# Kernel optimization log

Hardware: AMD Instinct MI355X
Metric: run time of the kernel (lower is better)

The kernel has to match this reference:

```python
import jax, jax.numpy as jnp
import numpy as np

B, CQ, CKV, H, W = 8, 256, 512, 64, 64
HKV, WKV = 32, 32
DQK = CQ // 8  # 32


def setup_inputs() -> dict:
    key = jax.random.key(0)
    ks = jax.random.split(key, 9)
    s = 0.05
    return {
        "query": jax.random.normal(ks[0], (B, CQ, H, W), jnp.float32),
        "key_value": jax.random.normal(ks[1], (B, CKV, HKV, WKV), jnp.float32),
        "Wq": jax.random.normal(ks[2], (DQK, CQ), jnp.float32) * s,
        "bq": jax.random.normal(ks[3], (DQK,), jnp.float32) * s,
        "Wk": jax.random.normal(ks[4], (DQK, CKV), jnp.float32) * s,
        "bk": jax.random.normal(ks[5], (DQK,), jnp.float32) * s,
        "Wv": jax.random.normal(ks[6], (CQ, CKV), jnp.float32) * s,
        "bv": jax.random.normal(ks[7], (CQ,), jnp.float32) * s,
        "gamma": jax.random.normal(ks[8], (1,), jnp.float32) * 0.5,
    }


def reference(query, key_value, Wq, bq, Wk, bk, Wv, bv, gamma):
    b, cq, h, w = query.shape
    n = h * w
    # bilinear resize of key_value to query's spatial size (align_corners=False
    # half-pixel convention, matching torch F.interpolate and jax.image.resize)
    kv = jax.image.resize(key_value, (b, key_value.shape[1], h, w), method="bilinear")
    # 1x1 convs are channel contractions
    q = jnp.einsum("bchw,dc->bdhw", query, Wq) + bq[None, :, None, None]   # [B,DQK,H,W]
    k = jnp.einsum("bchw,dc->bdhw", kv, Wk) + bk[None, :, None, None]      # [B,DQK,H,W]
    v = jnp.einsum("bchw,dc->bdhw", kv, Wv) + bv[None, :, None, None]      # [B,CQ,H,W]
    qf = q.reshape(b, -1, n)   # [B,DQK,N]
    kf = k.reshape(b, -1, n)   # [B,DQK,N]
    vf = v.reshape(b, -1, n)   # [B,CQ,N]
    energy = jnp.einsum("bdn,bdm->bnm", qf, kf)        # [B,N,N]
    attention = jax.nn.softmax(energy, axis=-1)
    out = jnp.einsum("bnm,bcm->bcn", attention, vf)     # [B,CQ,N]
    out = out.reshape(b, cq, h, w)
    return gamma[0] * out + query
```

## Files before the change

### kernel.cpp

```cpp
#include <hip/hip_runtime.h>

#define B_ 8
#define CQ_ 256
#define CKV_ 512
#define N_ 4096
#define DQK_ 32

typedef __bf16 bf16;
typedef __bf16 bf16x4 __attribute__((ext_vector_type(4)));
typedef __bf16 bf16x8 __attribute__((ext_vector_type(8)));
typedef float f32x4 __attribute__((ext_vector_type(4)));

__global__ void k_convert_w(const float* __restrict__ Wq, const float* __restrict__ Wk,
                            const float* __restrict__ Wv,
                            bf16* __restrict__ wq, bf16* __restrict__ wk, bf16* __restrict__ wv) {
    int i = blockIdx.x * 256 + threadIdx.x;
    if (i < 8192) wq[i] = (bf16)Wq[i];
    else if (i < 24576) wk[i - 8192] = (bf16)Wk[i - 8192];
    else if (i < 155648) wv[i - 24576] = (bf16)Wv[i - 24576];
}

__global__ __launch_bounds__(256) void k_resize(const float* __restrict__ kv, bf16* __restrict__ kvr) {
    const int yo = blockIdx.x;
    const int b  = blockIdx.y;
    const int tid = threadIdx.x;
    __shared__ float r0[64][33];
    __shared__ float r1[64][33];
    int ty = yo >> 1;
    int y0, y1; float wy0, wy1;
    if ((yo & 1) == 0) { y0 = ty > 0 ? ty - 1 : 0; y1 = ty; wy0 = 0.25f; wy1 = 0.75f; }
    else               { y0 = ty; y1 = ty < 31 ? ty + 1 : 31; wy0 = 0.75f; wy1 = 0.25f; }
    const int u_loc = tid & 63;
    const int xo_base = tid >> 6;
    for (int uc = 0; uc < CKV_; uc += 64) {
        __syncthreads();
        for (int i = 0; i < 8; ++i) {
            int idx = tid + i * 256;
            int u = idx >> 5, x = idx & 31;
            const float* src = kv + ((size_t)b * CKV_ + uc + u) * 1024 + x;
            r0[u][x] = src[y0 * 32];
            r1[u][x] = src[y1 * 32];
        }
        __syncthreads();
        for (int i = 0; i < 16; ++i) {
            int xo = xo_base + i * 4;
            int tx = xo >> 1;
            int xa, xb; float wxa, wxb;
            if ((xo & 1) == 0) { xa = tx > 0 ? tx - 1 : 0; xb = tx; wxa = 0.25f; wxb = 0.75f; }
            else               { xa = tx; xb = tx < 31 ? tx + 1 : 31; wxa = 0.75f; wxb = 0.25f; }
            float v0 = wxa * r0[u_loc][xa] + wxb * r0[u_loc][xb];
            float v1 = wxa * r1[u_loc][xa] + wxb * r1[u_loc][xb];
            float val = wy0 * v0 + wy1 * v1;
            kvr[((size_t)b * N_ + yo * 64 + xo) * CKV_ + uc + u_loc] = (bf16)val;
        }
    }
}

__global__ __launch_bounds__(256) void k_proj_q_fused(const float* __restrict__ query,
                                                      const bf16* __restrict__ W,
                                                      const float* __restrict__ bias,
                                                      bf16* __restrict__ qTb) {
    __shared__ bf16 tile[64][264];
    const int n0 = blockIdx.x * 64;
    const int b  = blockIdx.y;
    const int tid = threadIdx.x;
    const int xi = tid & 15, c0 = tid >> 4;
    for (int pass = 0; pass < 16; ++pass) {
        int c = c0 + pass * 16;
        const float4 v = *(const float4*)(query + ((size_t)b * CQ_ + c) * N_ + n0 + xi * 4);
        tile[xi * 4 + 0][c] = (bf16)v.x;
        tile[xi * 4 + 1][c] = (bf16)v.y;
        tile[xi * 4 + 2][c] = (bf16)v.z;
        tile[xi * 4 + 3][c] = (bf16)v.w;
    }
    __syncthreads();
    const int w = tid >> 6, lane = tid & 63;
    const int l16 = lane & 15, quad = lane >> 4;
    const int ct = w & 1, nh = w >> 1;
    f32x4 acc[2];
    acc[0] = (f32x4){0.f, 0.f, 0.f, 0.f}; acc[1] = (f32x4){0.f, 0.f, 0.f, 0.f};
    const bf16* aptr = W + (ct * 16 + l16) * CQ_ + quad * 8;
#pragma unroll
    for (int ks = 0; ks < 8; ++ks) {
        bf16x8 af = *(const bf16x8*)(aptr + ks * 32);
        for (int j = 0; j < 2; ++j) {
            bf16x8 bfv = *(const bf16x8*)&tile[nh * 32 + j * 16 + l16][ks * 32 + quad * 8];
            acc[j] = __builtin_amdgcn_mfma_f32_16x16x32_bf16(af, bfv, acc[j], 0, 0, 0);
        }
    }
    for (int j = 0; j < 2; ++j)
        for (int r = 0; r < 4; ++r) {
            int d = ct * 16 + quad * 4 + r;
            int n = n0 + nh * 32 + j * 16 + l16;
            qTb[((size_t)b * N_ + n) * DQK_ + d] = (bf16)(acc[j][r] + bias[d]);
        }
}

__global__ __launch_bounds__(256) void k_proj_k(const bf16* __restrict__ W,
                                                const float* __restrict__ bias,
                                                const bf16* __restrict__ Bm,
                                                bf16* __restrict__ outT) {
    const int mb = blockIdx.x * 128;
    const int b  = blockIdx.y;
    const int tid = threadIdx.x;
    const int w = tid >> 6, lane = tid & 63;
    const int l16 = lane & 15, quad = lane >> 4;
    const int ct = w & 1;
    const int mhalf = (w >> 1) * 64;
    f32x4 acc[4];
    for (int j = 0; j < 4; ++j) acc[j] = (f32x4){0.f, 0.f, 0.f, 0.f};
    const bf16* aptr  = W + (ct * 16 + l16) * CKV_ + quad * 8;
    const bf16* bbase = Bm + ((size_t)b * N_ + mb + mhalf) * CKV_ + quad * 8;
#pragma unroll
    for (int ks = 0; ks < 16; ++ks) {
        bf16x8 af = *(const bf16x8*)(aptr + ks * 32);
        for (int j = 0; j < 4; ++j) {
            bf16x8 bfv = *(const bf16x8*)(bbase + (size_t)(j * 16 + l16) * CKV_ + ks * 32);
            acc[j] = __builtin_amdgcn_mfma_f32_16x16x32_bf16(af, bfv, acc[j], 0, 0, 0);
        }
    }
    for (int j = 0; j < 4; ++j)
        for (int r = 0; r < 4; ++r) {
            int d = ct * 16 + quad * 4 + r;
            int m = mb + mhalf + j * 16 + l16;
            outT[((size_t)b * N_ + m) * DQK_ + d] = (bf16)(acc[j][r] + bias[d]);
        }
}

__global__ __launch_bounds__(256) void k_proj_v(const bf16* __restrict__ W,
                                                const float* __restrict__ bias,
                                                const bf16* __restrict__ Bm,
                                                bf16* __restrict__ vout) {
    const int mb = blockIdx.x * 64;
    const int b  = blockIdx.y;
    const int tid = threadIdx.x;
    const int w = tid >> 6, lane = tid & 63;
    const int l16 = lane & 15, quad = lane >> 4;
    f32x4 acc[4][4];
    for (int i = 0; i < 4; ++i) for (int j = 0; j < 4; ++j) acc[i][j] = (f32x4){0.f, 0.f, 0.f, 0.f};
    const bf16* bbase = Bm + ((size_t)b * N_ + mb) * CKV_ + quad * 8;
#pragma unroll 4
    for (int ks = 0; ks < 16; ++ks) {
        bf16x8 bfv[4];
        for (int j = 0; j < 4; ++j)
            bfv[j] = *(const bf16x8*)(bbase + (size_t)(j * 16 + l16) * CKV_ + ks * 32);
        for (int i = 0; i < 4; ++i) {
            bf16x8 af = *(const bf16x8*)(W + (size_t)((w * 4 + i) * 16 + l16) * CKV_ + ks * 32 + quad * 8);
            for (int j = 0; j < 4; ++j)
                acc[i][j] = __builtin_amdgcn_mfma_f32_16x16x32_bf16(af, bfv[j], acc[i][j], 0, 0, 0);
        }
    }
    for (int i = 0; i < 4; ++i)
        for (int r = 0; r < 4; ++r) {
            int c = (w * 4 + i) * 16 + quad * 4 + r;
            float bvs = bias[c];
            for (int j = 0; j < 4; ++j) {
                int m = mb + j * 16 + l16;
                vout[((size_t)b * CQ_ + c) * N_ + m] = (bf16)(acc[i][j][r] + bvs);
            }
        }
}

__global__ __launch_bounds__(256) void k_flash(const bf16* __restrict__ qT,
                                               const bf16* __restrict__ kT,
                                               const bf16* __restrict__ vv,
                                               const float* __restrict__ query,
                                               const float* __restrict__ gamma,
                                               float* __restrict__ out) {
    __shared__ bf16 P[4][64][72];
    const int b  = blockIdx.y;
    const int n0 = blockIdx.x * 64;
    const int tid = threadIdx.x;
    const int w = tid >> 6, lane = tid & 63;
    const int l16 = lane & 15, quad = lane >> 4;
    const int swz = l16 & 3;

    bf16x8 qfrag[4];
    for (int jn = 0; jn < 4; ++jn)
        qfrag[jn] = *(const bf16x8*)(qT + ((size_t)b * N_ + n0 + jn * 16 + l16) * DQK_ + quad * 8);

    f32x4 acc[4][4];
    for (int i = 0; i < 4; ++i) for (int j = 0; j < 4; ++j) acc[i][j] = (f32x4){0.f, 0.f, 0.f, 0.f};
    f32x4 lsum4[4];
    for (int j = 0; j < 4; ++j) lsum4[j] = (f32x4){0.f, 0.f, 0.f, 0.f};

    const bf16* kbase = kT + (size_t)b * N_ * DQK_;
    const bf16* vbase = vv + ((size_t)b * CQ_ + w * 64) * N_;
    bf16 (* __restrict__ Pw)[72] = P[w];

    for (int mt = 0; mt < 64; ++mt) {
        const int m0 = mt * 64;
        bf16x8 kf[4];
        for (int im = 0; im < 4; ++im)
            kf[im] = *(const bf16x8*)(kbase + (size_t)(m0 + im * 16 + l16) * DQK_ + quad * 8);
        bf16x8 vf[2][4];
        for (int ks = 0; ks < 2; ++ks)
            for (int i = 0; i < 4; ++i)
                vf[ks][i] = *(const bf16x8*)(vbase + (size_t)(i * 16 + l16) * N_ + m0 + ks * 32 + quad * 8);
        for (int jn = 0; jn < 4; ++jn) {
            for (int im = 0; im < 4; ++im) {
                f32x4 s = __builtin_amdgcn_mfma_f32_16x16x32_bf16(kf[im], qfrag[jn],
                                                                  (f32x4){0.f, 0.f, 0.f, 0.f}, 0, 0, 0);
                bf16x4 pk;
                for (int r = 0; r < 4; ++r) {
                    float p = __expf(s[r]);
                    lsum4[jn][r] += p;
                    pk[r] = (bf16)p;
                }
                *(bf16x4*)&Pw[jn * 16 + l16][((im ^ swz) << 4) + quad * 4] = pk;
            }
        }
        for (int ks = 0; ks < 2; ++ks) {
            bf16x8 pf[4];
            for (int j = 0; j < 4; ++j)
                pf[j] = *(const bf16x8*)&Pw[j * 16 + l16]
                            [((((ks << 1) | (quad >> 1)) ^ swz) << 4) + ((quad & 1) << 3)];
            for (int i = 0; i < 4; ++i)
                for (int j = 0; j < 4; ++j)
                    acc[i][j] = __builtin_amdgcn_mfma_f32_16x16x32_bf16(vf[ks][i], pf[j], acc[i][j], 0, 0, 0);
        }
    }
    float linv[4];
    for (int j = 0; j < 4; ++j) {
        float s = (lsum4[j][0] + lsum4[j][1]) + (lsum4[j][2] + lsum4[j][3]);
        s += __shfl_xor(s, 16);
        s += __shfl_xor(s, 32);
        linv[j] = 1.f / s;
    }
    const float g = gamma[0];
    for (int i = 0; i < 4; ++i)
        for (int r = 0; r < 4; ++r) {
            int c = w * 64 + i * 16 + quad * 4 + r;
            for (int j = 0; j < 4; ++j) {
                int n = n0 + j * 16 + l16;
                size_t idx = ((size_t)b * CQ_ + c) * N_ + n;
                out[idx] = g * acc[i][j][r] * linv[j] + query[idx];
            }
        }
}

extern "C" void kernel_launch(void* const* d_in, const int* in_sizes, int n_in,
                              void* d_out, int out_size, void* d_ws, size_t ws_size,
                              hipStream_t stream) {
    const float* query     = (const float*)d_in[0];
    const float* key_value = (const float*)d_in[1];
    const float* Wq = (const float*)d_in[2];
    const float* bq = (const float*)d_in[3];
    const float* Wk = (const float*)d_in[4];
    const float* bk = (const float*)d_in[5];
    const float* Wv = (const float*)d_in[6];
    const float* bv = (const float*)d_in[7];
    const float* gamma = (const float*)d_in[8];
    float* out = (float*)d_out;

    char* ws = (char*)d_ws;
    bf16* kvr  = (bf16*)(ws);
    bf16* vbuf = (bf16*)(ws + 33554432);
    bf16* qTb  = (bf16*)(ws + 50331648);
    bf16* kTb  = (bf16*)(ws + 52428800);
    bf16* wqb  = (bf16*)(ws + 54525952);
    bf16* wkb  = (bf16*)(ws + 54542336);
    bf16* wvb  = (bf16*)(ws + 54575104);

    k_convert_w<<<608, 256, 0, stream>>>(Wq, Wk, Wv, wqb, wkb, wvb);
    k_resize<<<dim3(64, 8), 256, 0, stream>>>(key_value, kvr);
    k_proj_q_fused<<<dim3(64, 8), 256, 0, stream>>>(query, wqb, bq, qTb);
    k_proj_k<<<dim3(32, 8), 256, 0, stream>>>(wkb, bk, kvr, kTb);
    k_proj_v<<<dim3(64, 8), 256, 0, stream>>>(wvb, bv, kvr, vbuf);
    k_flash<<<dim3(64, 8), 256, 0, stream>>>(qTb, kTb, vbuf, query, gamma, out);
}
```

Baseline: 345.0 us.

## Software-pipeline flash loop, fold log2e into Q, compute row sums via MFMA

Q is pre-scaled by log2(e) so the flash kernel can use the hardware exp2 instead of __expf. The main loop is software-pipelined: K and V loads for the next tile are issued early, and the P·V MFMAs for the previous tile overlap the QK/exp work of the current one. The softmax denominator is now accumulated with an extra MFMA against a ones vector instead of scalar adds and shuffles. The change also swizzles the LDS layout differently, swaps the grid so batch is the fast dimension, and sets launch bounds for two blocks per CU. In exchange it raises register pressure and sums the bf16-rounded probabilities rather than the fp32 values.

After: 345.6 us. No clear change (+0.2%).

```diff
diff --git a/kernel.cpp b/kernel.cpp
--- a/kernel.cpp
+++ b/kernel.cpp
@@ -88,11 +88,12 @@
             acc[j] = __builtin_amdgcn_mfma_f32_16x16x32_bf16(af, bfv, acc[j], 0, 0, 0);
         }
     }
+    const float LOG2E = 1.4426950408889634f;
     for (int j = 0; j < 2; ++j)
         for (int r = 0; r < 4; ++r) {
             int d = ct * 16 + quad * 4 + r;
             int n = n0 + nh * 32 + j * 16 + l16;
-            qTb[((size_t)b * N_ + n) * DQK_ + d] = (bf16)(acc[j][r] + bias[d]);
+            qTb[((size_t)b * N_ + n) * DQK_ + d] = (bf16)((acc[j][r] + bias[d]) * LOG2E);
         }
 }
 
@@ -161,72 +162,84 @@
         }
 }
 
-__global__ __launch_bounds__(256) void k_flash(const bf16* __restrict__ qT,
-                                               const bf16* __restrict__ kT,
-                                               const bf16* __restrict__ vv,
-                                               const float* __restrict__ query,
-                                               const float* __restrict__ gamma,
-                                               float* __restrict__ out) {
+__global__ __launch_bounds__(256, 2) void k_flash(const bf16* __restrict__ qT,
+                                                  const bf16* __restrict__ kT,
+                                                  const bf16* __restrict__ vv,
+                                                  const float* __restrict__ query,
+                                                  const float* __restrict__ gamma,
+                                                  float* __restrict__ out) {
     __shared__ bf16 P[4][64][72];
-    const int b  = blockIdx.y;
-    const int n0 = blockIdx.x * 64;
-    const int tid = threadIdx.x;
-    const int w = tid >> 6, lane = tid & 63;
-    const int l16 = lane & 15, quad = lane >> 4;
-    const int swz = l16 & 3;
+    const int b  = blockIdx.x;
+    const int n0 = blockIdx.y * 64;
+    const int tid = threadIdx.x;
+    const int w = tid >> 6, lane = tid & 63;
+    const int l16 = lane & 15, quad = lane >> 4;
+    const int swz = (l16 & 3) ^ ((l16 >> 3) << 1);
 
     bf16x8 qfrag[4];
     for (int jn = 0; jn < 4; ++jn)
         qfrag[jn] = *(const bf16x8*)(qT + ((size_t)b * N_ + n0 + jn * 16 + l16) * DQK_ + quad * 8);
 
+    const bf16 one = (bf16)1.0f;
+    const bf16x8 ones = {one, one, one, one, one, one, one, one};
+    const f32x4 zed = {0.f, 0.f, 0.f, 0.f};
+
     f32x4 acc[4][4];
-    for (int i = 0; i < 4; ++i) for (int j = 0; j < 4; ++j) acc[i][j] = (f32x4){0.f, 0.f, 0.f, 0.f};
-    f32x4 lsum4[4];
-    for (int j = 0; j < 4; ++j) lsum4[j] = (f32x4){0.f, 0.f, 0.f, 0.f};
-
-    const bf16* kbase = kT + (size_t)b * N_ * DQK_;
-    const bf16* vbase = vv + ((size_t)b * CQ_ + w * 64) * N_;
+    for (int i = 0; i < 4; ++i) for (int j = 0; j < 4; ++j) acc[i][j] = zed;
+    f32x4 accl[4];
+    for (int j = 0; j < 4; ++j) accl[j] = zed;
+
+    const bf16* kp = kT + ((size_t)b * N_ + l16) * DQK_ + quad * 8;
+    const bf16* vp[4];
+    for (int i = 0; i < 4; ++i)
+        vp[i] = vv + ((size_t)b * CQ_ + w * 64 + i * 16 + l16) * N_ + quad * 8;
+
     bf16 (* __restrict__ Pw)[72] = P[w];
 
+    bf16x8 kf[4], vf[2][4], pf[2][4];
+    for (int im = 0; im < 4; ++im) kf[im] = *(const bf16x8*)(kp + im * 16 * DQK_);
+    kp += 64 * DQK_;
+
     for (int mt = 0; mt < 64; ++mt) {
-        const int m0 = mt * 64;
-        bf16x8 kf[4];
-        for (int im = 0; im < 4; ++im)
-            kf[im] = *(const bf16x8*)(kbase + (size_t)(m0 + im * 16 + l16) * DQK_ + quad * 8);
-        bf16x8 vf[2][4];
+        if (mt)
+            for (int ks = 0; ks < 2; ++ks)
+                for (int j = 0; j < 4; ++j)
+                    pf[ks][j] = *(const bf16x8*)&Pw[j * 16 + l16]
+                                    [((((ks << 1) | (quad >> 1)) ^ swz) << 4) + ((quad & 1) << 3)];
+        for (int jn = 0; jn < 4; ++jn)
+            for (int im = 0; im < 4; ++im) {
+                f32x4 s = __builtin_amdgcn_mfma_f32_16x16x32_bf16(kf[im], qfrag[jn], zed, 0, 0, 0);
+                bf16x4 pk;
+                for (int r = 0; r < 4; ++r) pk[r] = (bf16)__builtin_amdgcn_exp2f(s[r]);
+                *(bf16x4*)&Pw[jn * 16 + l16][((im ^ swz) << 4) + quad * 4] = pk;
+            }
+        for (int im = 0; im < 4; ++im) kf[im] = *(const bf16x8*)(kp + im * 16 * DQK_);
+        kp += 64 * DQK_;
+        if (mt)
+            for (int ks = 0; ks < 2; ++ks)
+                for (int j = 0; j < 4; ++j) {
+                    accl[j] = __builtin_amdgcn_mfma_f32_16x16x32_bf16(ones, pf[ks][j], accl[j], 0, 0, 0);
+                    for (int i = 0; i < 4; ++i)
+                        acc[i][j] = __builtin_amdgcn_mfma_f32_16x16x32_bf16(vf[ks][i], pf[ks][j], acc[i][j], 0, 0, 0);
+                }
         for (int ks = 0; ks < 2; ++ks)
             for (int i = 0; i < 4; ++i)
-                vf[ks][i] = *(const bf16x8*)(vbase + (size_t)(i * 16 + l16) * N_ + m0 + ks * 32 + quad * 8);
-        for (int jn = 0; jn < 4; ++jn) {
-            for (int im = 0; im < 4; ++im) {
-                f32x4 s = __builtin_amdgcn_mfma_f32_16x16x32_bf16(kf[im], qfrag[jn],
-                                                                  (f32x4){0.f, 0.f, 0.f, 0.f}, 0, 0, 0);
-                bf16x4 pk;
-                for (int r = 0; r < 4; ++r) {
-                    float p = __expf(s[r]);
-                    lsum4[jn][r] += p;
-                    pk[r] = (bf16)p;
-                }
-                *(bf16x4*)&Pw[jn * 16 + l16][((im ^ swz) << 4) + quad * 4] = pk;
-            }
-        }
-        for (int ks = 0; ks < 2; ++ks) {
-            bf16x8 pf[4];
-            for (int j = 0; j < 4; ++j)
-                pf[j] = *(const bf16x8*)&Pw[j * 16 + l16]
+                vf[ks][i] = *(const bf16x8*)(vp[i] + ks * 32);
+        for (int i = 0; i < 4; ++i) vp[i] += 64;
+    }
+    for (int ks = 0; ks < 2; ++ks)
+        for (int j = 0; j < 4; ++j)
+            pf[ks][j] = *(const bf16x8*)&Pw[j * 16 + l16]
                             [((((ks << 1) | (quad >> 1)) ^ swz) << 4) + ((quad & 1) << 3)];
+    for (int ks = 0; ks < 2; ++ks)
+        for (int j = 0; j < 4; ++j) {
+            accl[j] = __builtin_amdgcn_mfma_f32_16x16x32_bf16(ones, pf[ks][j], accl[j], 0, 0, 0);
             for (int i = 0; i < 4; ++i)
-                for (int j = 0; j < 4; ++j)
-                    acc[i][j] = __builtin_amdgcn_mfma_f32_16x16x32_bf16(vf[ks][i], pf[j], acc[i][j], 0, 0, 0);
-        }
-    }
+                acc[i][j] = __builtin_amdgcn_mfma_f32_16x16x32_bf16(vf[ks][i], pf[ks][j], acc[i][j], 0, 0, 0);
+        }
+
     float linv[4];
-    for (int j = 0; j < 4; ++j) {
-        float s = (lsum4[j][0] + lsum4[j][1]) + (lsum4[j][2] + lsum4[j][3]);
-        s += __shfl_xor(s, 16);
-        s += __shfl_xor(s, 32);
-        linv[j] = 1.f / s;
-    }
+    for (int j = 0; j < 4; ++j) linv[j] = 1.f / accl[j][0];
     const float g = gamma[0];
     for (int i = 0; i < 4; ++i)
         for (int r = 0; r < 4; ++r) {
@@ -267,5 +280,5 @@
     k_proj_q_fused<<<dim3(64, 8), 256, 0, stream>>>(query, wqb, bq, qTb);
     k_proj_k<<<dim3(32, 8), 256, 0, stream>>>(wkb, bk, kvr, kTb);
     k_proj_v<<<dim3(64, 8), 256, 0, stream>>>(wvb, bv, kvr, vbuf);
-    k_flash<<<dim3(64, 8), 256, 0, stream>>>(qTb, kTb, vbuf, query, gamma, out);
-}
+    k_flash<<<dim3(8, 64), 256, 0, stream>>>(qTb, kTb, vbuf, query, gamma, out);
+}
```
